# Kernel tuning notes

Hardware: AMD Instinct MI355X
Metric: run time of the kernel (lower is better)

The kernel has to match this reference:

```python
import jax, jax.numpy as jnp
import numpy as np
import math

D_MODEL = 1024
N_HEADS = 16
D_HEAD = D_MODEL // N_HEADS
NUM_BUCKETS = 32
MAX_DISTANCE = 128


def _relative_position_bucket(relative_position):
    # bidirectional T5-style bucketing
    num_buckets = NUM_BUCKETS // 2
    buckets = (relative_position > 0).astype(jnp.int32) * num_buckets
    rp = jnp.abs(relative_position)
    max_exact = num_buckets // 2
    is_small = rp < max_exact
    rpf = jnp.maximum(rp, 1).astype(jnp.float32)  # avoid log(0); masked by is_small
    rp_large = max_exact + (
        jnp.log(rpf / max_exact) / math.log(MAX_DISTANCE / max_exact) * (num_buckets - max_exact)
    ).astype(jnp.int32)
    rp_large = jnp.minimum(rp_large, num_buckets - 1)
    return buckets + jnp.where(is_small, rp, rp_large)


def _compute_bias(q_len, k_len, rel_emb):
    context_pos = jnp.arange(q_len, dtype=jnp.int32)[:, None]
    memory_pos = jnp.arange(k_len, dtype=jnp.int32)[None, :]
    rp_bucket = _relative_position_bucket(memory_pos - context_pos)  # [Tq, Tk]
    values = rel_emb[rp_bucket]                 # [Tq, Tk, H]
    return jnp.transpose(values, (2, 0, 1))[None]  # [1, H, Tq, Tk]


def setup_inputs() -> dict:
    key = jax.random.key(0)
    ks = jax.random.split(key, 8)
    B, T = 4, 2048
    return {
        "query": jax.random.normal(ks[0], (B, T, D_MODEL), dtype=jnp.float32),
        "key": jax.random.normal(ks[1], (B, T, D_MODEL), dtype=jnp.float32),
        "value": jax.random.normal(ks[2], (B, T, D_MODEL), dtype=jnp.float32),
        "Wq": jax.random.normal(ks[3], (D_MODEL, D_MODEL), dtype=jnp.float32) * 0.02,
        "Wk": jax.random.normal(ks[4], (D_MODEL, D_MODEL), dtype=jnp.float32) * 0.02,
        "Wv": jax.random.normal(ks[5], (D_MODEL, D_MODEL), dtype=jnp.float32) * 0.02,
        "Wo": jax.random.normal(ks[6], (D_MODEL, D_MODEL), dtype=jnp.float32) * 0.02,
        "rel_emb": jax.random.normal(ks[7], (NUM_BUCKETS, N_HEADS), dtype=jnp.float32) * 0.02,
    }


def reference(query, key, value, Wq, Wk, Wv, Wo, rel_emb):
    B, Tq, _ = query.shape
    Tk = key.shape[1]
    # torch nn.Linear(bias=False): y = x @ W.T
    q = (query @ Wq.T).reshape(B, Tq, N_HEADS, D_HEAD).transpose(0, 2, 1, 3)  # [B,H,Tq,Dh]
    k = (key @ Wk.T).reshape(B, Tk, N_HEADS, D_HEAD).transpose(0, 2, 1, 3)
    v = (value @ Wv.T).reshape(B, Tk, N_HEADS, D_HEAD).transpose(0, 2, 1, 3)
    scores = jnp.einsum("bhqd,bhkd->bhqk", q, k) / math.sqrt(D_HEAD)  # [B,H,Tq,Tk]
    position_bias = _compute_bias(Tq, Tk, rel_emb)
    scores = scores + position_bias
    attn = jax.nn.softmax(scores, axis=-1)
    out = jnp.einsum("bhqk,bhkd->bhqd", attn, v)
    out = out.transpose(0, 2, 1, 3).reshape(B, Tq, D_MODEL)
    out = out @ Wo.T
    return out, position_bias
```

## Files before the change

kernel.cpp:

```cpp
#include <hip/hip_runtime.h>

typedef _Float16 half8 __attribute__((ext_vector_type(8)));
typedef _Float16 half4 __attribute__((ext_vector_type(4)));
typedef float f32x4 __attribute__((ext_vector_type(4)));

#define DEV __device__ __forceinline__

DEV f32x4 mfma16(half8 a, half8 b, f32x4 c) {
  return __builtin_amdgcn_mfma_f32_16x16x32_f16(a, b, c, 0, 0, 0);
}

DEV void load_lds16(const void* g, void* l) {
  __builtin_amdgcn_global_load_lds((const __attribute__((address_space(1))) void*)g,
                                   (__attribute__((address_space(3))) void*)l, 16, 0, 0);
}

DEV int t5_bucket(int delta) {
  int b = (delta > 0) ? 16 : 0;
  int rp = delta < 0 ? -delta : delta;
  if (rp < 8) return b + rp;
  float lg = logf((float)rp * 0.125f);
  int large = 8 + (int)(lg / 2.772588722239781f * 8.0f);
  if (large > 15) large = 15;
  return b + large;
}

DEV float bias_val(const float* rel, int n, int h) {
  return rel[t5_bucket(n - 2047) * 16 + h];
}

__global__ __launch_bounds__(256) void prep_kernel(
    const float* __restrict__ q, const float* __restrict__ k, const float* __restrict__ v,
    const float* __restrict__ wq, const float* __restrict__ wk, const float* __restrict__ wv,
    const float* __restrict__ wo, const float* __restrict__ rel,
    _Float16* __restrict__ Xh, _Float16* __restrict__ W3h, _Float16* __restrict__ Woh,
    _Float16* __restrict__ BiasH, float* __restrict__ Bf) {
  unsigned u = blockIdx.x * 256u + threadIdx.x;
  if (u < 6291456u) {
    unsigned p = u / 2097152u, r = u - p * 2097152u;
    const float4* s = (const float4*)(p == 0 ? q : p == 1 ? k : v);
    float4 x = s[r];
    half4 hv = {(_Float16)x.x, (_Float16)x.y, (_Float16)x.z, (_Float16)x.w};
    *(half4*)(Xh + (size_t)p * 8388608u + (size_t)r * 4u) = hv;
  } else if (u < 7340032u) {
    unsigned t = u - 6291456u;
    const float4* s;
    _Float16* d;
    if (t < 786432u) {
      unsigned p = t / 262144u, r = t - p * 262144u;
      s = (const float4*)(p == 0 ? wq : p == 1 ? wk : wv) + r;
      d = W3h + (size_t)p * 1048576u + (size_t)r * 4u;
    } else {
      unsigned r = t - 786432u;
      s = (const float4*)wo + r;
      d = Woh + (size_t)r * 4u;
    }
    float4 x = *s;
    half4 hv = {(_Float16)x.x, (_Float16)x.y, (_Float16)x.z, (_Float16)x.w};
    *(half4*)d = hv;
  } else {
    unsigned t = u - 7340032u;
    int h = (int)(t >> 12), n = (int)(t & 4095u);
    Bf[h * 4096 + n] = (n <= 4094) ? bias_val(rel, n, h) : 0.f;
    half4 hv;
#pragma unroll
    for (int j = 0; j < 4; j++) {
      float bv = (n + j <= 4094) ? bias_val(rel, n + j, h) * 1.4426950408889634f : 0.f;
      hv[j] = (_Float16)bv;
    }
    *(half4*)(BiasH + (size_t)(h * 4096 + n) * 4u) = hv;
  }
}

template <int MODE>
__global__ __launch_bounds__(256) void gemm128(
    const _Float16* __restrict__ A, const _Float16* __restrict__ B,
    _Float16* __restrict__ D0, _Float16* __restrict__ D1, _Float16* __restrict__ D2,
    float* __restrict__ F) {
  __shared__ _Float16 Asm[128 * 64];
  __shared__ _Float16 Bsm[128 * 64];
  const int tid = threadIdx.x;
  const int w = tid >> 6, L = tid & 63;
  const int g = L >> 4, c15 = L & 15;
  const int m0 = blockIdx.y * 128, n0 = blockIdx.x * 128;
  const int z = blockIdx.z;
  const _Float16* Ab = A + ((size_t)z * 8192 + m0) * 1024;
  const _Float16* Bb = B + ((size_t)z * 1024 + n0) * 1024;
  f32x4 acc[4][4] = {};
  const int mw = (w & 1) * 64, nw = (w >> 1) * 64;
  const int wbase = tid & ~63;
  for (int k0 = 0; k0 < 1024; k0 += 64) {
    __syncthreads();
#pragma unroll
    for (int c = 0; c < 4; c++) {
      int i = c * 256 + tid;
      int row = i >> 3, pc = i & 7;
      int lc = pc ^ ((row >> 1) & 7);
      load_lds16(Ab + (size_t)row * 1024 + k0 + lc * 8, Asm + (c * 256 + wbase) * 8);
      load_lds16(Bb + (size_t)row * 1024 + k0 + lc * 8, Bsm + (c * 256 + wbase) * 8);
    }
    __builtin_amdgcn_s_waitcnt(0);
    __syncthreads();
#pragma unroll
    for (int kc = 0; kc < 2; kc++) {
      half8 af[4], bf[4];
#pragma unroll
      for (int t = 0; t < 4; t++) {
        int rowA = mw + t * 16 + c15;
        int pcA = (kc * 4 + g) ^ ((rowA >> 1) & 7);
        af[t] = *(const half8*)(Asm + rowA * 64 + pcA * 8);
        int rowB = nw + t * 16 + c15;
        int pcB = (kc * 4 + g) ^ ((rowB >> 1) & 7);
        bf[t] = *(const half8*)(Bsm + rowB * 64 + pcB * 8);
      }
#pragma unroll
      for (int mt = 0; mt < 4; mt++)
#pragma unroll
        for (int nt = 0; nt < 4; nt++)
          acc[mt][nt] = mfma16(bf[nt], af[mt], acc[mt][nt]);
    }
  }
  if (MODE == 0) {
    float scale = (z == 0) ? 0.18033688011112042f : 1.0f;
    _Float16* dst = (z == 0) ? D0 : (z == 1) ? D1 : D2;
#pragma unroll
    for (int mt = 0; mt < 4; mt++) {
      int m = m0 + mw + mt * 16 + c15;
      int bb = m >> 11, t = m & 2047;
#pragma unroll
      for (int nt = 0; nt < 4; nt++) {
        int n = n0 + nw + nt * 16 + g * 4;
        half4 hv;
#pragma unroll
        for (int r = 0; r < 4; r++) hv[r] = (_Float16)(acc[mt][nt][r] * scale);
        *(half4*)(dst + (((size_t)bb * 16 + (n >> 6)) * 2048 + t) * 64 + (n & 63)) = hv;
      }
    }
  } else {
#pragma unroll
    for (int mt = 0; mt < 4; mt++) {
      int m = m0 + mw + mt * 16 + c15;
#pragma unroll
      for (int nt = 0; nt < 4; nt++) {
        int n = n0 + nw + nt * 16 + g * 4;
        float4 fv = make_float4(acc[mt][nt][0], acc[mt][nt][1], acc[mt][nt][2], acc[mt][nt][3]);
        *(float4*)(F + (size_t)m * 1024 + n) = fv;
      }
    }
  }
}

__global__ __launch_bounds__(256) void transpose_v(const _Float16* __restrict__ V,
                                                   _Float16* __restrict__ Vt) {
  int bh = blockIdx.z * 16 + blockIdx.y;
  const _Float16* Vb = V + (size_t)bh * 2048 * 64;
  _Float16* Vtb = Vt + (size_t)bh * 80 * 2048;
  int tid = threadIdx.x;
  if (blockIdx.x == 32) {
    _Float16 one = (_Float16)1.0f, zero = (_Float16)0.0f;
#pragma unroll
    for (int j = 0; j < 16; j++) {
      half8 vv;
#pragma unroll
      for (int e = 0; e < 8; e++) vv[e] = (j == 0) ? one : zero;
      *(half8*)(Vtb + (size_t)(64 + j) * 2048 + tid * 8) = vv;
    }
    return;
  }
  __shared__ _Float16 tileS[64][64];
  int t0 = blockIdx.x * 64;
#pragma unroll
  for (int c = 0; c < 2; c++) {
    int i = c * 256 + tid;
    int row = i >> 3, col = (i & 7) * 8;
    half8 vv = *(const half8*)(Vb + (size_t)(t0 + row) * 64 + col);
    int xr = 8 * ((col >> 3) & 7);
#pragma unroll
    for (int j = 0; j < 8; j++) tileS[col + j][row ^ xr] = vv[j];
  }
  __syncthreads();
  int d = tid >> 2, c = (tid & 3) * 16;
  int xr = 8 * ((d >> 3) & 7);
  half8 o0 = *(const half8*)(&tileS[d][c ^ xr]);
  half8 o1 = *(const half8*)(&tileS[d][(c + 8) ^ xr]);
  *(half8*)(Vtb + (size_t)d * 2048 + t0 + c) = o0;
  *(half8*)(Vtb + (size_t)d * 2048 + t0 + c + 8) = o1;
}

__global__ __launch_bounds__(256, 2) void flash_attn(
    const _Float16* __restrict__ Q, const _Float16* __restrict__ K,
    const _Float16* __restrict__ Vt, const _Float16* __restrict__ BiasH,
    _Float16* __restrict__ AO) {
  __shared__ _Float16 Kst[2][64 * 64];
  __shared__ _Float16 Vst[2][80 * 64];
  __shared__ half4 biasS[2176];
  __shared__ _Float16 pS[4][32][72];
  const int b = blockIdx.z, h = blockIdx.x, qb = blockIdx.y * 128;
  const int bh = b * 16 + h;
  const _Float16* Qb = Q + (size_t)bh * 2048 * 64;
  const _Float16* Kb = K + (size_t)bh * 2048 * 64;
  const _Float16* Vtb = Vt + (size_t)bh * 80 * 2048;
  const int tid = threadIdx.x, w = tid >> 6, L = tid & 63;
  const int g = L >> 4, c15 = L & 15;
  const int wbase = tid & ~63;
  const int idx0 = 1920 - qb;

  auto stage = [&](int buf, int kk) {
#pragma unroll
    for (int c = 0; c < 2; c++) {
      int i = c * 256 + tid;
      int row = i >> 3, pc = i & 7, lc = pc ^ ((row >> 1) & 7);
      load_lds16(Kb + (size_t)(kk + row) * 64 + lc * 8, &Kst[buf][(c * 256 + wbase) * 8]);
    }
#pragma unroll
    for (int c = 0; c < 2; c++) {
      int i = c * 256 + tid;
      int row = i >> 3, pc = i & 7, lc = pc ^ ((row >> 1) & 7);
      load_lds16(Vtb + (size_t)row * 2048 + kk + lc * 8, &Vst[buf][(c * 256 + wbase) * 8]);
    }
    if (tid < 128) {
      int i = 512 + tid;
      int row = i >> 3, pc = i & 7, lc = pc ^ ((row >> 1) & 7);
      load_lds16(Vtb + (size_t)row * 2048 + kk + lc * 8, &Vst[buf][(512 + wbase) * 8]);
    }
  };

  stage(0, 0);
  for (int i = tid; i < 2176; i += 256)
    biasS[i] = *(const half4*)(BiasH + (size_t)(h * 4096 + idx0 + i) * 4u);
  half8 qf[2][2];
#pragma unroll
  for (int r2 = 0; r2 < 2; r2++)
#pragma unroll
    for (int kc = 0; kc < 2; kc++)
      qf[r2][kc] =
          *(const half8*)(Qb + (size_t)(qb + w * 32 + r2 * 16 + c15) * 64 + kc * 32 + g * 8);
  f32x4 O[2][5] = {};
  __builtin_amdgcn_s_waitcnt(0);
  __syncthreads();

  for (int kt = 0; kt < 32; kt++) {
    const int cur = kt & 1, nxt = cur ^ 1;
    if (kt < 31) stage(nxt, (kt + 1) * 64);
    half8 kf[4][2];
#pragma unroll
    for (int nt = 0; nt < 4; nt++)
#pragma unroll
      for (int kc = 0; kc < 2; kc++) {
        int row = nt * 16 + c15;
        int pc = (kc * 4 + g) ^ ((row >> 1) & 7);
        kf[nt][kc] = *(const half8*)(&Kst[cur][row * 64 + pc * 8]);
      }
    half8 vf[5][2];
#pragma unroll
    for (int dt = 0; dt < 5; dt++)
#pragma unroll
      for (int kc = 0; kc < 2; kc++) {
        int row = dt * 16 + c15;
        int pc = (kc * 4 + g) ^ ((row >> 1) & 7);
        vf[dt][kc] = *(const half8*)(&Vst[cur][row * 64 + pc * 8]);
      }
    f32x4 S[2][4];
#pragma unroll
    for (int nt = 0; nt < 4; nt++)
#pragma unroll
      for (int r2 = 0; r2 < 2; r2++) {
        f32x4 z = {};
        f32x4 s0 = mfma16(kf[nt][0], qf[r2][0], z);
        S[r2][nt] = mfma16(kf[nt][1], qf[r2][1], s0);
      }
#pragma unroll
    for (int r2 = 0; r2 < 2; r2++) {
      int qloc = w * 32 + r2 * 16 + c15;
#pragma unroll
      for (int nt = 0; nt < 4; nt++) {
        half4 bv = biasS[kt * 64 + nt * 16 + g * 4 + 127 - qloc];
        half4 pv;
#pragma unroll
        for (int r = 0; r < 4; r++) {
          float p = __builtin_amdgcn_exp2f(S[r2][nt][r] + (float)bv[r]);
          pv[r] = (_Float16)p;
        }
        *(half4*)(&pS[w][r2 * 16 + c15][nt * 16 + g * 4]) = pv;
      }
    }
    __builtin_amdgcn_s_waitcnt(0xc07f);
#pragma unroll
    for (int r2 = 0; r2 < 2; r2++) {
      half8 pa0 = *(const half8*)(&pS[w][r2 * 16 + c15][g * 8]);
      half8 pa1 = *(const half8*)(&pS[w][r2 * 16 + c15][32 + g * 8]);
#pragma unroll
      for (int dt = 0; dt < 5; dt++) {
        O[r2][dt] = mfma16(vf[dt][0], pa0, O[r2][dt]);
        O[r2][dt] = mfma16(vf[dt][1], pa1, O[r2][dt]);
      }
    }
    __builtin_amdgcn_s_waitcnt(0);
    __syncthreads();
  }
#pragma unroll
  for (int r2 = 0; r2 < 2; r2++) {
    float linv = 1.0f / __shfl(O[r2][4][0], c15, 64);
    int qg = qb + w * 32 + r2 * 16 + c15;
    _Float16* dst = AO + ((size_t)(b * 2048 + qg)) * 1024 + h * 64;
#pragma unroll
    for (int dt = 0; dt < 4; dt++) {
      half4 ov;
#pragma unroll
      for (int r = 0; r < 4; r++) ov[r] = (_Float16)(O[r2][dt][r] * linv);
      *(half4*)(dst + dt * 16 + g * 4) = ov;
    }
  }
}

__global__ __launch_bounds__(256) void bias_out_k(const float* __restrict__ Bf,
                                                  float4* __restrict__ out2) {
  unsigned u = blockIdx.x * 256u + threadIdx.x;
  int hh = (int)(u >> 20);
  unsigned rem = u & 1048575u;
  int i = (int)(rem >> 9);
  int j4 = (int)(rem & 511u) * 4;
  const float* p = Bf + hh * 4096 + j4 - i + 2047;
  out2[u] = make_float4(p[0], p[1], p[2], p[3]);
}

extern "C" void kernel_launch(void* const* d_in, const int* in_sizes, int n_in,
                              void* d_out, int out_size, void* d_ws, size_t ws_size,
                              hipStream_t stream) {
  const float* q = (const float*)d_in[0];
  const float* k = (const float*)d_in[1];
  const float* v = (const float*)d_in[2];
  const float* wq = (const float*)d_in[3];
  const float* wk = (const float*)d_in[4];
  const float* wv = (const float*)d_in[5];
  const float* wo = (const float*)d_in[6];
  const float* rel = (const float*)d_in[7];

  _Float16* Xh = (_Float16*)d_ws;
  _Float16* W3h = Xh + 3u * 8388608u;
  _Float16* Woh = W3h + 3u * 1048576u;
  _Float16* Qh = Woh + 1048576u;
  _Float16* Kh = Qh + 8388608u;
  _Float16* Vh = Kh + 8388608u;
  _Float16* Vth = Vh + 8388608u;
  _Float16* AOh = Vth + 10485760u;
  _Float16* BiasH = AOh + 8388608u;
  float* Bf = (float*)(BiasH + 262144u);
  float* outp = (float*)d_out;

  prep_kernel<<<28928, 256, 0, stream>>>(q, k, v, wq, wk, wv, wo, rel, Xh, W3h, Woh, BiasH, Bf);
  gemm128<0><<<dim3(8, 64, 3), 256, 0, stream>>>(Xh, W3h, Qh, Kh, Vh, nullptr);
  transpose_v<<<dim3(33, 16, 4), 256, 0, stream>>>(Vh, Vth);
  flash_attn<<<dim3(16, 16, 4), 256, 0, stream>>>(Qh, Kh, Vth, BiasH, AOh);
  gemm128<1><<<dim3(8, 64, 1), 256, 0, stream>>>(AOh, Woh, nullptr, nullptr, nullptr, outp);
  bias_out_k<<<65536, 256, 0, stream>>>(Bf, (float4*)(outp + 8388608u));
}
```

Before: 622.6 us.

## Double flash-attention query tile per block and swap GEMM grid raster order

Each flash-attention block now covers 256 query rows (64 per wave) instead of 128, so each staged K/V tile is reused across twice as many queries. The P·V product is split into two 32-key halves with a smaller P scratch buffer, so V fragments are loaded per half and register pressure stays bounded. The GEMM grid swaps x/y so consecutive blocks walk along M instead of N, which changes cache locality of the weight and activation tiles. The trade-off is a grid half as large for attention (512 blocks), more accumulator registers per wave that may hurt occupancy, and extra LDS round trips.

```diff
diff --git a/kernel.cpp b/kernel.cpp
--- a/kernel.cpp
+++ b/kernel.cpp
@@ -82,7 +82,7 @@
   const int tid = threadIdx.x;
   const int w = tid >> 6, L = tid & 63;
   const int g = L >> 4, c15 = L & 15;
-  const int m0 = blockIdx.y * 128, n0 = blockIdx.x * 128;
+  const int m0 = blockIdx.x * 128, n0 = blockIdx.y * 128;
   const int z = blockIdx.z;
   const _Float16* Ab = A + ((size_t)z * 8192 + m0) * 1024;
   const _Float16* Bb = B + ((size_t)z * 1024 + n0) * 1024;
@@ -193,9 +193,9 @@
     _Float16* __restrict__ AO) {
   __shared__ _Float16 Kst[2][64 * 64];
   __shared__ _Float16 Vst[2][80 * 64];
-  __shared__ half4 biasS[2176];
-  __shared__ _Float16 pS[4][32][72];
-  const int b = blockIdx.z, h = blockIdx.x, qb = blockIdx.y * 128;
+  __shared__ half4 biasS[2304];
+  __shared__ _Float16 pS[4][64][40];
+  const int b = blockIdx.z, h = blockIdx.x, qb = blockIdx.y * 256;
   const int bh = b * 16 + h;
   const _Float16* Qb = Q + (size_t)bh * 2048 * 64;
   const _Float16* Kb = K + (size_t)bh * 2048 * 64;
@@ -203,7 +203,7 @@
   const int tid = threadIdx.x, w = tid >> 6, L = tid & 63;
   const int g = L >> 4, c15 = L & 15;
   const int wbase = tid & ~63;
-  const int idx0 = 1920 - qb;
+  const int idx0 = 1792 - qb;
 
   auto stage = [&](int buf, int kk) {
 #pragma unroll
@@ -226,16 +226,16 @@
   };
 
   stage(0, 0);
-  for (int i = tid; i < 2176; i += 256)
+  for (int i = tid; i < 2304; i += 256)
     biasS[i] = *(const half4*)(BiasH + (size_t)(h * 4096 + idx0 + i) * 4u);
-  half8 qf[2][2];
-#pragma unroll
-  for (int r2 = 0; r2 < 2; r2++)
+  half8 qf[4][2];
+#pragma unroll
+  for (int r2 = 0; r2 < 4; r2++)
 #pragma unroll
     for (int kc = 0; kc < 2; kc++)
       qf[r2][kc] =
-          *(const half8*)(Qb + (size_t)(qb + w * 32 + r2 * 16 + c15) * 64 + kc * 32 + g * 8);
-  f32x4 O[2][5] = {};
+          *(const half8*)(Qb + (size_t)(qb + w * 64 + r2 * 16 + c15) * 64 + kc * 32 + g * 8);
+  f32x4 O[4][5] = {};
   __builtin_amdgcn_s_waitcnt(0);
   __syncthreads();
 
@@ -251,57 +251,77 @@
         int pc = (kc * 4 + g) ^ ((row >> 1) & 7);
         kf[nt][kc] = *(const half8*)(&Kst[cur][row * 64 + pc * 8]);
       }
-    half8 vf[5][2];
-#pragma unroll
-    for (int dt = 0; dt < 5; dt++)
-#pragma unroll
-      for (int kc = 0; kc < 2; kc++) {
-        int row = dt * 16 + c15;
-        int pc = (kc * 4 + g) ^ ((row >> 1) & 7);
-        vf[dt][kc] = *(const half8*)(&Vst[cur][row * 64 + pc * 8]);
-      }
-    f32x4 S[2][4];
+    half8 vf[5];
+#pragma unroll
+    for (int dt = 0; dt < 5; dt++) {
+      int row = dt * 16 + c15;
+      int pc = g ^ ((row >> 1) & 7);
+      vf[dt] = *(const half8*)(&Vst[cur][row * 64 + pc * 8]);
+    }
+    f32x4 S[4][4];
 #pragma unroll
     for (int nt = 0; nt < 4; nt++)
 #pragma unroll
-      for (int r2 = 0; r2 < 2; r2++) {
+      for (int r2 = 0; r2 < 4; r2++) {
         f32x4 z = {};
         f32x4 s0 = mfma16(kf[nt][0], qf[r2][0], z);
         S[r2][nt] = mfma16(kf[nt][1], qf[r2][1], s0);
       }
 #pragma unroll
-    for (int r2 = 0; r2 < 2; r2++) {
-      int qloc = w * 32 + r2 * 16 + c15;
-#pragma unroll
-      for (int nt = 0; nt < 4; nt++) {
-        half4 bv = biasS[kt * 64 + nt * 16 + g * 4 + 127 - qloc];
+    for (int r2 = 0; r2 < 4; r2++) {
+      int qloc = w * 64 + r2 * 16 + c15;
+#pragma unroll
+      for (int nt2 = 0; nt2 < 2; nt2++) {
+        half4 bv = biasS[kt * 64 + nt2 * 16 + g * 4 + 255 - qloc];
         half4 pv;
 #pragma unroll
-        for (int r = 0; r < 4; r++) {
-          float p = __builtin_amdgcn_exp2f(S[r2][nt][r] + (float)bv[r]);
-          pv[r] = (_Float16)p;
-        }
-        *(half4*)(&pS[w][r2 * 16 + c15][nt * 16 + g * 4]) = pv;
+        for (int r = 0; r < 4; r++)
+          pv[r] = (_Float16)__builtin_amdgcn_exp2f(S[r2][nt2][r] + (float)bv[r]);
+        *(half4*)(&pS[w][r2 * 16 + c15][nt2 * 16 + g * 4]) = pv;
       }
     }
     __builtin_amdgcn_s_waitcnt(0xc07f);
-#pragma unroll
-    for (int r2 = 0; r2 < 2; r2++) {
-      half8 pa0 = *(const half8*)(&pS[w][r2 * 16 + c15][g * 8]);
-      half8 pa1 = *(const half8*)(&pS[w][r2 * 16 + c15][32 + g * 8]);
-#pragma unroll
-      for (int dt = 0; dt < 5; dt++) {
-        O[r2][dt] = mfma16(vf[dt][0], pa0, O[r2][dt]);
-        O[r2][dt] = mfma16(vf[dt][1], pa1, O[r2][dt]);
-      }
-    }
+    half8 pa[4];
+#pragma unroll
+    for (int r2 = 0; r2 < 4; r2++) pa[r2] = *(const half8*)(&pS[w][r2 * 16 + c15][g * 8]);
+    half8 vg[5];
+#pragma unroll
+    for (int dt = 0; dt < 5; dt++) {
+      int row = dt * 16 + c15;
+      int pc = (4 + g) ^ ((row >> 1) & 7);
+      vg[dt] = *(const half8*)(&Vst[cur][row * 64 + pc * 8]);
+    }
+#pragma unroll
+    for (int r2 = 0; r2 < 4; r2++)
+#pragma unroll
+      for (int dt = 0; dt < 5; dt++) O[r2][dt] = mfma16(vf[dt], pa[r2], O[r2][dt]);
+#pragma unroll
+    for (int r2 = 0; r2 < 4; r2++) {
+      int qloc = w * 64 + r2 * 16 + c15;
+#pragma unroll
+      for (int nt2 = 0; nt2 < 2; nt2++) {
+        half4 bv = biasS[kt * 64 + 32 + nt2 * 16 + g * 4 + 255 - qloc];
+        half4 pv;
+#pragma unroll
+        for (int r = 0; r < 4; r++)
+          pv[r] = (_Float16)__builtin_amdgcn_exp2f(S[r2][2 + nt2][r] + (float)bv[r]);
+        *(half4*)(&pS[w][r2 * 16 + c15][nt2 * 16 + g * 4]) = pv;
+      }
+    }
+    __builtin_amdgcn_s_waitcnt(0xc07f);
+#pragma unroll
+    for (int r2 = 0; r2 < 4; r2++) pa[r2] = *(const half8*)(&pS[w][r2 * 16 + c15][g * 8]);
+#pragma unroll
+    for (int r2 = 0; r2 < 4; r2++)
+#pragma unroll
+      for (int dt = 0; dt < 5; dt++) O[r2][dt] = mfma16(vg[dt], pa[r2], O[r2][dt]);
     __builtin_amdgcn_s_waitcnt(0);
     __syncthreads();
   }
 #pragma unroll
-  for (int r2 = 0; r2 < 2; r2++) {
+  for (int r2 = 0; r2 < 4; r2++) {
     float linv = 1.0f / __shfl(O[r2][4][0], c15, 64);
-    int qg = qb + w * 32 + r2 * 16 + c15;
+    int qg = qb + w * 64 + r2 * 16 + c15;
     _Float16* dst = AO + ((size_t)(b * 2048 + qg)) * 1024 + h * 64;
 #pragma unroll
     for (int dt = 0; dt < 4; dt++) {
@@ -349,9 +369,9 @@
   float* outp = (float*)d_out;
 
   prep_kernel<<<28928, 256, 0, stream>>>(q, k, v, wq, wk, wv, wo, rel, Xh, W3h, Woh, BiasH, Bf);
-  gemm128<0><<<dim3(8, 64, 3), 256, 0, stream>>>(Xh, W3h, Qh, Kh, Vh, nullptr);
+  gemm128<0><<<dim3(64, 8, 3), 256, 0, stream>>>(Xh, W3h, Qh, Kh, Vh, nullptr);
   transpose_v<<<dim3(33, 16, 4), 256, 0, stream>>>(Vh, Vth);
-  flash_attn<<<dim3(16, 16, 4), 256, 0, stream>>>(Qh, Kh, Vth, BiasH, AOh);
-  gemm128<1><<<dim3(8, 64, 1), 256, 0, stream>>>(AOh, Woh, nullptr, nullptr, nullptr, outp);
+  flash_attn<<<dim3(16, 8, 4), 256, 0, stream>>>(Qh, Kh, Vth, BiasH, AOh);
+  gemm128<1><<<dim3(64, 8, 1), 256, 0, stream>>>(AOh, Woh, nullptr, nullptr, nullptr, outp);
   bias_out_k<<<65536, 256, 0, stream>>>(Bf, (float4*)(outp + 8388608u));
 }
```

Result: faster. 596.8 us (-4.1%).
